# Kernel tuning notes

Hardware: AMD Instinct MI355X
Metric: run time of the kernel (lower is better)

Reference implementation:

```python
import jax, jax.numpy as jnp
import numpy as np

N = 50000      # nodes
E = 1600000    # edges (avg degree 32)
G = 128        # graphs in batch
NE = 5         # spectral supports (edge_attr channels)
NIN = 16       # input node features
H = 64         # nout1 hidden width
NCLS = 6
BN_EPS = 1e-5


def setup_inputs() -> dict:
    key = jax.random.key(0)
    ks = jax.random.split(key, 12)
    s = 0.1  # weight init scale
    x = jax.random.normal(ks[0], (N, NIN), dtype=jnp.float32)
    edge_index = jax.random.randint(ks[1], (2, E), 0, N, dtype=jnp.int32)
    edge_attr = jax.random.normal(ks[2], (E, NE), dtype=jnp.float32)
    # sorted segment ids covering all G graphs (non-empty segments)
    batch = ((jnp.arange(N, dtype=jnp.int32) * G) // N).astype(jnp.int32)
    W1 = jax.random.normal(ks[3], (NE, NIN, H), dtype=jnp.float32) * s
    W2 = jax.random.normal(ks[4], (NE, H, H), dtype=jnp.float32) * s
    W3 = jax.random.normal(ks[5], (NE, H, H), dtype=jnp.float32) * s
    W4 = jax.random.normal(ks[6], (NE, H, H), dtype=jnp.float32) * s
    b1 = jnp.zeros((H,), jnp.float32)
    b2 = jnp.zeros((H,), jnp.float32)
    b3 = jnp.zeros((H,), jnp.float32)
    b4 = jnp.zeros((H,), jnp.float32)
    bn_gamma = jnp.ones((2 * H,), jnp.float32)
    bn_beta = jnp.zeros((2 * H,), jnp.float32)
    bn_mean = jax.random.normal(ks[7], (2 * H,), dtype=jnp.float32)
    bn_var = jax.random.uniform(ks[8], (2 * H,), dtype=jnp.float32) + 0.5
    fc_w = jax.random.normal(ks[9], (2 * H, NCLS), dtype=jnp.float32) * s
    fc_b = jnp.zeros((NCLS,), jnp.float32)
    return {"x": x, "edge_index": edge_index, "edge_attr": edge_attr,
            "batch": batch, "W1": W1, "b1": b1, "W2": W2, "b2": b2,
            "W3": W3, "b3": b3, "W4": W4, "b4": b4,
            "bn_gamma": bn_gamma, "bn_beta": bn_beta,
            "bn_mean": bn_mean, "bn_var": bn_var,
            "fc_w": fc_w, "fc_b": fc_b}


def spect_conv(x, src, dst, edge_attr, W, b):
    # SpectConv(selfconn=False): out = sum_k scatter_add(edge_attr[:,k]*x[src] -> dst) @ W[k] + b
    xs = x[src]  # [E, F] gather
    n = x.shape[0]
    out = jnp.zeros((n, W.shape[2]), x.dtype)
    for k in range(W.shape[0]):  # K=5 spectral supports
        h = jax.ops.segment_sum(edge_attr[:, k:k + 1] * xs, dst, num_segments=n)
        out = out + h @ W[k]
    return out + b


def reference(x, edge_index, edge_attr, batch, W1, b1, W2, b2, W3, b3, W4, b4,
              bn_gamma, bn_beta, bn_mean, bn_var, fc_w, fc_b):
    src, dst = edge_index[0], edge_index[1]
    h = jax.nn.relu(spect_conv(x, src, dst, edge_attr, W1, b1))
    h = jax.nn.relu(spect_conv(h, src, dst, edge_attr, W2, b2))
    h = jax.nn.relu(spect_conv(h, src, dst, edge_attr, W3, b3))
    h = jax.nn.relu(spect_conv(h, src, dst, edge_attr, W4, b4))
    pooled = jnp.concatenate([
        jax.ops.segment_sum(h, batch, num_segments=G),
        jax.ops.segment_max(h, batch, num_segments=G)], axis=1)  # [G, 2H]
    bn = (pooled - bn_mean) * jax.lax.rsqrt(bn_var + BN_EPS) * bn_gamma + bn_beta
    return jax.nn.log_softmax(bn @ fc_w + fc_b, axis=1)
```

## Files before the change

### kernel.cpp

```cpp
#include <hip/hip_runtime.h>


#define Nn   50000
#define Ne   1600000
#define Gg   128
#define NEk  5
#define NINf 16
#define NCLSo 6
#define NB   196
#define RBK  128
#define CHK  (Ne / RBK)

using short8 = __attribute__((ext_vector_type(8))) short;
using f32x4  = __attribute__((ext_vector_type(4))) float;
using f32x2  = __attribute__((ext_vector_type(2))) float;
using uint4v = __attribute__((ext_vector_type(4))) unsigned;

__device__ __forceinline__ float2 bf2u(unsigned u) {
    return make_float2(__uint_as_float(u << 16), __uint_as_float(u & 0xffff0000u));
}
__device__ __forceinline__ unsigned f2bf(float a, float b) {
    unsigned ua = __float_as_uint(a), ub = __float_as_uint(b);
    ua += 0x7fffu + ((ua >> 16) & 1u);
    ub += 0x7fffu + ((ub >> 16) & 1u);
    return (ua >> 16) | (ub & 0xffff0000u);
}
__device__ __forceinline__ unsigned short f2bf1(float a) {
    unsigned ua = __float_as_uint(a);
    ua += 0x7fffu + ((ua >> 16) & 1u);
    return (unsigned short)(ua >> 16);
}

__device__ __forceinline__ f32x2 fma2s(float a, f32x2 x, f32x2 c) {
#if __has_builtin(__builtin_elementwise_fma)
    f32x2 av; av.x = a; av.y = a;
    return __builtin_elementwise_fma(av, x, c);
#else
    c.x = fmaf(a, x.x, c.x); c.y = fmaf(a, x.y, c.y);
    return c;
#endif
}


__global__ void k_pad_x(const float* __restrict__ x, unsigned* __restrict__ h0) {
    int i = blockIdx.x * 256 + threadIdx.x;
    if (i >= Nn * 32) return;
    int n = i >> 5, p = i & 31;
    int f0 = 2 * p;
    float v0 = (f0 < NINf) ? x[n * NINf + f0] : 0.f;
    float v1 = (f0 + 1 < NINf) ? x[n * NINf + f0 + 1] : 0.f;
    h0[i] = f2bf(v0, v1);
}

__global__ void k_pad_w1(const float* __restrict__ W1, float* __restrict__ W1p) {
    int i = blockIdx.x * 256 + threadIdx.x;
    if (i >= NEk * 64 * 64) return;
    int h = i & 63, f = (i >> 6) & 63, k = i >> 12;
    W1p[i] = (f < NINf) ? W1[(k * NINf + f) * 64 + h] : 0.f;
}

__global__ void k_pack_b(const float* __restrict__ W, unsigned short* __restrict__ bhi,
                         unsigned short* __restrict__ blo) {
    int i = blockIdx.x * 256 + threadIdx.x;
    if (i >= 20480) return;
    int j = i & 7, lane = (i >> 3) & 63, t2 = i >> 9;
    int nt = t2 / 10, kstep = t2 - nt * 10;
    int k = kstep * 32 + (lane >> 4) * 8 + j;
    int col = nt * 16 + (lane & 15);
    float v = W[k * 64 + col];
    unsigned short hi = f2bf1(v);
    float fhi = __uint_as_float(((unsigned)hi) << 16);
    bhi[i] = hi;
    blo[i] = f2bf1(v - fhi);
}

__global__ __launch_bounds__(1024) void k_rankhist(
    const int* __restrict__ ei, unsigned short* __restrict__ lrank,
    unsigned short* __restrict__ cnt ) {
    __shared__ unsigned hist[12500];
    int b = blockIdx.x, t = threadIdx.x;
    int e0 = b * CHK;
    for (int w = t; w < 12500; w += 1024) hist[w] = 0;
    __syncthreads();
    for (int i = t; i < CHK; i += 1024) {
        int d = ei[Ne + e0 + i];
        unsigned sh = 8u * (unsigned)(d & 3);
        unsigned old = atomicAdd(&hist[d >> 2], 1u << sh);
        lrank[e0 + i] = (unsigned short)((old >> sh) & 0xffu);
    }
    __syncthreads();
    unsigned* co = (unsigned*)(cnt + (size_t)b * Nn);
    for (int w = t; w < 12500; w += 1024) {
        unsigned hv = hist[w];
        co[2 * w]     = (hv & 0xffu) | ((hv >> 8) & 0xffu) << 16;
        co[2 * w + 1] = ((hv >> 16) & 0xffu) | (hv >> 24) << 16;
    }
}

__global__ void k_colscan(unsigned short* __restrict__ cnt, int* __restrict__ deg) {
    int d = blockIdx.x * 256 + threadIdx.x;
    if (d >= Nn) return;
    int s = 0;
#pragma unroll 4
    for (int b = 0; b < RBK; ++b) {
        int t = cnt[(size_t)b * Nn + d];
        cnt[(size_t)b * Nn + d] = (unsigned short)s;
        s += t;
    }
    deg[d] = s;
}


__global__ void k_blocksum(const int* __restrict__ deg, int* __restrict__ bsum) {
    __shared__ int l[256];
    int t = threadIdx.x;
    int i = blockIdx.x * 256 + t;
    l[t] = (i < Nn) ? deg[i] : 0;
    __syncthreads();
    for (int off = 128; off > 0; off >>= 1) {
        if (t < off) l[t] += l[t + off];
        __syncthreads();
    }
    if (t == 0) bsum[blockIdx.x] = l[0];
}

__global__ void k_scanpart(const int* __restrict__ bsum, int* __restrict__ boff) {
    __shared__ int l[256];
    int t = threadIdx.x;
    int v = (t < NB) ? bsum[t] : 0;
    l[t] = v;
    __syncthreads();
    for (int off = 1; off < 256; off <<= 1) {
        int u = (t >= off) ? l[t - off] : 0;
        __syncthreads();
        l[t] += u;
        __syncthreads();
    }
    if (t < NB) boff[t] = l[t] - v;
}

__global__ void k_scanfinal(const int* __restrict__ deg, const int* __restrict__ boff,
                            int* __restrict__ rowstart) {
    __shared__ int l[256];
    int t = threadIdx.x;
    int i = blockIdx.x * 256 + t;
    int v = (i < Nn) ? deg[i] : 0;
    l[t] = v;
    __syncthreads();
    for (int off = 1; off < 256; off <<= 1) {
        int u = (t >= off) ? l[t - off] : 0;
        __syncthreads();
        l[t] += u;
        __syncthreads();
    }
    if (i <= Nn) rowstart[i] = boff[blockIdx.x] + l[t] - v;
}

__global__ __launch_bounds__(256) void k_place(
    const int* __restrict__ ei, const float* __restrict__ eattr,
    const int* __restrict__ rowstart,
    const unsigned short* __restrict__ lrank,
    const unsigned short* __restrict__ cnt,
    unsigned* __restrict__ recs ) {
    int e = (blockIdx.x * 256 + threadIdx.x) * 4;
    if (e >= Ne) return;
    int b = e / CHK;
    const unsigned short* cb = cnt + (size_t)b * Nn;

    int4 dv = *(const int4*)(ei + Ne + e);
    int4 sv = *(const int4*)(ei + e);
    ushort4 lr = *(const ushort4*)(lrank + e);
    union { float4 v4[5]; float f[20]; } a;
#pragma unroll
    for (int q = 0; q < 5; ++q) a.v4[q] = *(const float4*)(eattr + (size_t)e * 5 + q * 4);

    int d[4] = { dv.x, dv.y, dv.z, dv.w };
    int s[4] = { sv.x, sv.y, sv.z, sv.w };
    unsigned short r4[4] = { lr.x, lr.y, lr.z, lr.w };
    int pos[4];
#pragma unroll
    for (int j = 0; j < 4; ++j)
        pos[j] = rowstart[d[j]] + cb[d[j]] + r4[j];
#pragma unroll
    for (int j = 0; j < 4; ++j) {
        uint4v rr;
        rr.x = (unsigned)s[j];
        rr.y = f2bf(a.f[5 * j],     a.f[5 * j + 1]);
        rr.z = f2bf(a.f[5 * j + 2], a.f[5 * j + 3]);
        rr.w = f2bf(a.f[5 * j + 4], 0.f);
        __builtin_nontemporal_store(rr, (uint4v*)(recs + (size_t)pos[j] * 4));
    }
}

__global__ void k_bounds(const int* __restrict__ batch, int* __restrict__ sg,
                         int* __restrict__ eg) {
    int n = blockIdx.x * 256 + threadIdx.x;
    if (n >= Nn) return;
    int g = batch[n];
    if (n == 0) sg[g] = 0;
    else {
        int gp = batch[n - 1];
        if (gp != g) { sg[g] = n; eg[gp] = n; }
    }
    if (n == Nn - 1) eg[g] = Nn;
}

#define SPAD 41
__global__ __launch_bounds__(256) void k_layer32(
    const unsigned* __restrict__ hin, const int* __restrict__ rowstart,
    const uint4* __restrict__ recs, const unsigned short* __restrict__ bhi,
    const unsigned short* __restrict__ blo, const float* __restrict__ bias,
    unsigned* __restrict__ outh) {
    __shared__ uint4 smem[32 * SPAD];
    unsigned* aggw = (unsigned*)smem;
    int t = threadIdx.x;
    int lane = t & 63, wave = t >> 6;
    int l = lane & 31, half = lane >> 5;
    int blk = blockIdx.x;

#pragma unroll 1
    for (int ni = 0; ni < 8; ++ni) {
        int row = wave * 8 + ni;
        int node = blk * 32 + row;
        if (node >= Nn) node = Nn - 1;
        node = __builtin_amdgcn_readfirstlane(node);
        int beg = rowstart[node], end = rowstart[node + 1];
        f32x2 c0 = {0.f, 0.f}, c1 = c0, c2 = c0, c3 = c0, c4 = c0;
        int ee = beg;
#define EDGE(E) { \
    uint4 r = recs[(E)]; \
    unsigned hx = hin[(size_t)(int)r.x * 32 + l]; \
    f32x2 xv; xv.x = __uint_as_float(hx << 16); xv.y = __uint_as_float(hx & 0xffff0000u); \
    float A0 = __uint_as_float(r.y << 16), A1 = __uint_as_float(r.y & 0xffff0000u); \
    float A2 = __uint_as_float(r.z << 16), A3 = __uint_as_float(r.z & 0xffff0000u); \
    float A4 = __uint_as_float(r.w << 16); \
    c0 = fma2s(A0, xv, c0); c1 = fma2s(A1, xv, c1); \
    c2 = fma2s(A2, xv, c2); c3 = fma2s(A3, xv, c3); \
    c4 = fma2s(A4, xv, c4); }
        for (; ee + 8 <= end; ee += 8) {
            EDGE(ee + half) EDGE(ee + 2 + half) EDGE(ee + 4 + half) EDGE(ee + 6 + half)
        }
        for (; ee + 2 <= end; ee += 2) { EDGE(ee + half) }
        if (ee < end) { if (half == 0) { EDGE(ee) } }
#undef EDGE
        c0.x += __shfl(c0.x, lane ^ 32); c0.y += __shfl(c0.y, lane ^ 32);
        c1.x += __shfl(c1.x, lane ^ 32); c1.y += __shfl(c1.y, lane ^ 32);
        c2.x += __shfl(c2.x, lane ^ 32); c2.y += __shfl(c2.y, lane ^ 32);
        c3.x += __shfl(c3.x, lane ^ 32); c3.y += __shfl(c3.y, lane ^ 32);
        c4.x += __shfl(c4.x, lane ^ 32); c4.y += __shfl(c4.y, lane ^ 32);
        if (half == 0) {
            unsigned* o = aggw + row * (SPAD * 4) + l;
            o[0]   = f2bf(c0.x, c0.y);
            o[32]  = f2bf(c1.x, c1.y);
            o[64]  = f2bf(c2.x, c2.y);
            o[96]  = f2bf(c3.x, c3.y);
            o[128] = f2bf(c4.x, c4.y);
        }
    }
    __syncthreads();

    int m = lane & 15, quad = lane >> 4;
    f32x4 acc0 = {0.f, 0.f, 0.f, 0.f}, acc1 = acc0;
    const uint4* ar0 = smem + m * SPAD + quad;
    const uint4* ar1 = smem + (16 + m) * SPAD + quad;
    const size_t bbase = (size_t)wave * 5120;
#pragma unroll 2
    for (int ks = 0; ks < 10; ++ks) {
        short8 a0 = *(const short8*)(ar0 + ks * 4);
        short8 a1 = *(const short8*)(ar1 + ks * 4);
        size_t bb = bbase + ((size_t)ks * 64 + lane) * 8;
        short8 h = *(const short8*)(bhi + bb);
        short8 lo = *(const short8*)(blo + bb);
        acc0 = __builtin_amdgcn_mfma_f32_16x16x32_bf16(a0, h,  acc0, 0, 0, 0);
        acc0 = __builtin_amdgcn_mfma_f32_16x16x32_bf16(a0, lo, acc0, 0, 0, 0);
        acc1 = __builtin_amdgcn_mfma_f32_16x16x32_bf16(a1, h,  acc1, 0, 0, 0);
        acc1 = __builtin_amdgcn_mfma_f32_16x16x32_bf16(a1, lo, acc1, 0, 0, 0);
    }
    __syncthreads();

    float* Cs = (float*)smem;
#pragma unroll
    for (int r = 0; r < 4; ++r) {
        int base = (quad * 4 + r) * 72 + wave * 16 + m;
        Cs[base]            = acc0[r];
        Cs[base + 16 * 72]  = acc1[r];
    }
    __syncthreads();

    {
        int row = t >> 3, grp = t & 7;
        int node = blk * 32 + row;
        if (node < Nn) {
            const float* cr = Cs + row * 72;
            unsigned o[4];
#pragma unroll
            for (int j = 0; j < 4; ++j) {
                int pp = grp * 4 + j;
                float v0 = fmaxf(cr[2 * pp]     + bias[2 * pp],     0.f);
                float v1 = fmaxf(cr[2 * pp + 1] + bias[2 * pp + 1], 0.f);
                o[j] = f2bf(v0, v1);
            }
            *(uint4*)(outh + (size_t)node * 32 + grp * 4) =
                make_uint4(o[0], o[1], o[2], o[3]);
        }
    }
}


__global__ __launch_bounds__(256) void k_pool(const unsigned* __restrict__ h,
                                              const int* __restrict__ sg,
                                              const int* __restrict__ eg,
                                              float* __restrict__ pooled) {
    __shared__ float2 ls[256], lm[256];
    int g = blockIdx.x, t = threadIdx.x;
    int p = t & 31, q = t >> 5;
    int s = sg[g], e = eg[g];
    float2 sum = {0.f, 0.f}, mx = {0.f, 0.f};
    for (int n = s + q; n < e; n += 8) {
        float2 v = bf2u(h[(size_t)n * 32 + p]);
        sum.x += v.x; sum.y += v.y;
        mx.x = fmaxf(mx.x, v.x); mx.y = fmaxf(mx.y, v.y);
    }
    ls[t] = sum; lm[t] = mx;
    __syncthreads();
    if (t < 32) {
        float2 ss = ls[t], mm = lm[t];
        for (int i = 1; i < 8; ++i) {
            float2 a = ls[t + i * 32], b = lm[t + i * 32];
            ss.x += a.x; ss.y += a.y;
            mm.x = fmaxf(mm.x, b.x); mm.y = fmaxf(mm.y, b.y);
        }
        pooled[g * 128 + 2 * t]          = ss.x;
        pooled[g * 128 + 2 * t + 1]      = ss.y;
        pooled[g * 128 + 64 + 2 * t]     = mm.x;
        pooled[g * 128 + 64 + 2 * t + 1] = mm.y;
    }
}

__global__ void k_head(const float* __restrict__ pooled, const float* __restrict__ gamma,
                       const float* __restrict__ beta, const float* __restrict__ mean,
                       const float* __restrict__ var, const float* __restrict__ fcw,
                       const float* __restrict__ fcb, float* __restrict__ out) {
    __shared__ float y[128];
    __shared__ float lg[8];
    int g = blockIdx.x, c = threadIdx.x;
    float p = pooled[g * 128 + c];
    y[c] = (p - mean[c]) * rsqrtf(var[c] + 1e-5f) * gamma[c] + beta[c];
    __syncthreads();
    if (c < NCLSo) {
        float l = fcb[c];
        for (int i = 0; i < 128; ++i) l += y[i] * fcw[i * NCLSo + c];
        lg[c] = l;
    }
    __syncthreads();
    if (c == 0) {
        float m = lg[0];
        for (int j = 1; j < NCLSo; ++j) m = fmaxf(m, lg[j]);
        float se = 0.f;
        for (int j = 0; j < NCLSo; ++j) se += expf(lg[j] - m);
        float lse = m + logf(se);
        for (int j = 0; j < NCLSo; ++j) out[g * NCLSo + j] = lg[j] - lse;
    }
}


static inline size_t rup(size_t x) { return (x + 255) & ~(size_t)255; }

extern "C" void kernel_launch(void* const* d_in, const int* in_sizes, int n_in,
                              void* d_out, int out_size, void* d_ws, size_t ws_size,
                              hipStream_t stream) {
    const float* x     = (const float*)d_in[0];
    const int*   ei    = (const int*)d_in[1];
    const float* eattr = (const float*)d_in[2];
    const int*   batch = (const int*)d_in[3];
    const float* W1    = (const float*)d_in[4];
    const float* b1    = (const float*)d_in[5];
    const float* W2    = (const float*)d_in[6];
    const float* b2    = (const float*)d_in[7];
    const float* W3    = (const float*)d_in[8];
    const float* b3    = (const float*)d_in[9];
    const float* W4    = (const float*)d_in[10];
    const float* b4    = (const float*)d_in[11];
    const float* gamma = (const float*)d_in[12];
    const float* beta  = (const float*)d_in[13];
    const float* mean  = (const float*)d_in[14];
    const float* var   = (const float*)d_in[15];
    const float* fcw   = (const float*)d_in[16];
    const float* fcb   = (const float*)d_in[17];
    float* out = (float*)d_out;

    char* p = (char*)d_ws;
    auto take = [&](size_t bytes) { char* r = p; p += rup(bytes); return r; };
    int*            deg      = (int*)take((size_t)(Nn + 1) * 4);
    unsigned short* cnt      = (unsigned short*)take((size_t)RBK * Nn * 2);
    unsigned short* lrank    = (unsigned short*)take((size_t)Ne * 2);
    int*            rowstart = (int*)take((size_t)(Nn + 1) * 4);
    int*            bsum     = (int*)take((size_t)NB * 4);
    int*            boff     = (int*)take((size_t)NB * 4);
    uint4*          recs     = (uint4*)take((size_t)Ne * 16);
    unsigned*       hA       = (unsigned*)take((size_t)Nn * 32 * 4);
    unsigned*       hB       = (unsigned*)take((size_t)Nn * 32 * 4);
    float*          W1p      = (float*)take((size_t)NEk * 64 * 64 * 4);
    unsigned short* bhiA     = (unsigned short*)take((size_t)4 * 20480 * 2);
    unsigned short* bloA     = (unsigned short*)take((size_t)4 * 20480 * 2);
    float*          pooled   = (float*)take((size_t)Gg * 128 * 4);
    int*            sg       = (int*)take((size_t)Gg * 4);
    int*            eg       = (int*)take((size_t)Gg * 4);

    k_rankhist<<<RBK, 1024, 0, stream>>>(ei, lrank, cnt);
    k_pad_x<<<(Nn * 32 + 255) / 256, 256, 0, stream>>>(x, hA);
    k_pad_w1<<<(NEk * 64 * 64 + 255) / 256, 256, 0, stream>>>(W1, W1p);
    k_pack_b<<<80, 256, 0, stream>>>(W1p, bhiA,             bloA);
    k_pack_b<<<80, 256, 0, stream>>>(W2,  bhiA + 20480,     bloA + 20480);
    k_pack_b<<<80, 256, 0, stream>>>(W3,  bhiA + 2 * 20480, bloA + 2 * 20480);
    k_pack_b<<<80, 256, 0, stream>>>(W4,  bhiA + 3 * 20480, bloA + 3 * 20480);
    k_colscan<<<NB, 256, 0, stream>>>(cnt, deg);
    k_blocksum<<<NB, 256, 0, stream>>>(deg, bsum);
    k_scanpart<<<1, 256, 0, stream>>>(bsum, boff);
    k_scanfinal<<<NB, 256, 0, stream>>>(deg, boff, rowstart);
    k_place<<<(Ne / 4 + 255) / 256, 256, 0, stream>>>(ei, eattr, rowstart, lrank, cnt,
                                                      (unsigned*)recs);
    k_bounds<<<(Nn + 255) / 256, 256, 0, stream>>>(batch, sg, eg);

    const float* bs[4] = { b1, b2, b3, b4 };
    unsigned* cur = hA;
    unsigned* nxt = hB;
    for (int L = 0; L < 4; ++L) {
        k_layer32<<<(Nn + 31) / 32, 256, 0, stream>>>(
            cur, rowstart, recs, bhiA + (size_t)L * 20480, bloA + (size_t)L * 20480,
            bs[L], nxt);
        unsigned* tmp = cur; cur = nxt; nxt = tmp;
    }

    k_pool<<<Gg, 256, 0, stream>>>(cur, sg, eg, pooled);
    k_head<<<Gg, 128, 0, stream>>>(pooled, gamma, beta, mean, var, fcw, fcb, out);
}
```

Baseline: 554.0 us.

## Split fused layer kernel into separate aggregate and transform kernels

Result: faster. 455.9 us (median of 2 runs) (-17.7%).

```diff
diff --git a/kernel.cpp b/kernel.cpp
--- a/kernel.cpp
+++ b/kernel.cpp
@@ -14,7 +14,6 @@
 using short8 = __attribute__((ext_vector_type(8))) short;
 using f32x4  = __attribute__((ext_vector_type(4))) float;
 using f32x2  = __attribute__((ext_vector_type(2))) float;
-using uint4v = __attribute__((ext_vector_type(4))) unsigned;
 
 __device__ __forceinline__ float2 bf2u(unsigned u) {
     return make_float2(__uint_as_float(u << 16), __uint_as_float(u & 0xffff0000u));
@@ -156,40 +155,23 @@
     if (i <= Nn) rowstart[i] = boff[blockIdx.x] + l[t] - v;
 }
 
-__global__ __launch_bounds__(256) void k_place(
-    const int* __restrict__ ei, const float* __restrict__ eattr,
-    const int* __restrict__ rowstart,
-    const unsigned short* __restrict__ lrank,
-    const unsigned short* __restrict__ cnt,
-    unsigned* __restrict__ recs ) {
-    int e = (blockIdx.x * 256 + threadIdx.x) * 4;
+__global__ void k_place(const int* __restrict__ ei, const float* __restrict__ eattr,
+                        const int* __restrict__ rowstart,
+                        const unsigned short* __restrict__ lrank,
+                        const unsigned short* __restrict__ cnt,
+                        uint4* __restrict__ recs) {
+    int e = blockIdx.x * 256 + threadIdx.x;
     if (e >= Ne) return;
+    int d = ei[Ne + e];
     int b = e / CHK;
-    const unsigned short* cb = cnt + (size_t)b * Nn;
-
-    int4 dv = *(const int4*)(ei + Ne + e);
-    int4 sv = *(const int4*)(ei + e);
-    ushort4 lr = *(const ushort4*)(lrank + e);
-    union { float4 v4[5]; float f[20]; } a;
-#pragma unroll
-    for (int q = 0; q < 5; ++q) a.v4[q] = *(const float4*)(eattr + (size_t)e * 5 + q * 4);
-
-    int d[4] = { dv.x, dv.y, dv.z, dv.w };
-    int s[4] = { sv.x, sv.y, sv.z, sv.w };
-    unsigned short r4[4] = { lr.x, lr.y, lr.z, lr.w };
-    int pos[4];
-#pragma unroll
-    for (int j = 0; j < 4; ++j)
-        pos[j] = rowstart[d[j]] + cb[d[j]] + r4[j];
-#pragma unroll
-    for (int j = 0; j < 4; ++j) {
-        uint4v rr;
-        rr.x = (unsigned)s[j];
-        rr.y = f2bf(a.f[5 * j],     a.f[5 * j + 1]);
-        rr.z = f2bf(a.f[5 * j + 2], a.f[5 * j + 3]);
-        rr.w = f2bf(a.f[5 * j + 4], 0.f);
-        __builtin_nontemporal_store(rr, (uint4v*)(recs + (size_t)pos[j] * 4));
-    }
+    int pos = rowstart[d] + cnt[(size_t)b * Nn + d] + lrank[e];
+    const float* a = eattr + (size_t)e * 5;
+    uint4 rr;
+    rr.x = (unsigned)ei[e];
+    rr.y = f2bf(a[0], a[1]);
+    rr.z = f2bf(a[2], a[3]);
+    rr.w = f2bf(a[4], 0.f);
+    recs[pos] = rr;
 }
 
 __global__ void k_bounds(const int* __restrict__ batch, int* __restrict__ sg,
@@ -205,28 +187,16 @@
     if (n == Nn - 1) eg[g] = Nn;
 }
 
-#define SPAD 41
-__global__ __launch_bounds__(256) void k_layer32(
+
+__global__ __launch_bounds__(256) void k_aggregate(
     const unsigned* __restrict__ hin, const int* __restrict__ rowstart,
-    const uint4* __restrict__ recs, const unsigned short* __restrict__ bhi,
-    const unsigned short* __restrict__ blo, const float* __restrict__ bias,
-    unsigned* __restrict__ outh) {
-    __shared__ uint4 smem[32 * SPAD];
-    unsigned* aggw = (unsigned*)smem;
-    int t = threadIdx.x;
-    int lane = t & 63, wave = t >> 6;
+    const uint4* __restrict__ recs, unsigned* __restrict__ agg) {
+    int lane = threadIdx.x & 63;
     int l = lane & 31, half = lane >> 5;
-    int blk = blockIdx.x;
-
-#pragma unroll 1
-    for (int ni = 0; ni < 8; ++ni) {
-        int row = wave * 8 + ni;
-        int node = blk * 32 + row;
-        if (node >= Nn) node = Nn - 1;
-        node = __builtin_amdgcn_readfirstlane(node);
-        int beg = rowstart[node], end = rowstart[node + 1];
-        f32x2 c0 = {0.f, 0.f}, c1 = c0, c2 = c0, c3 = c0, c4 = c0;
-        int ee = beg;
+    int node = __builtin_amdgcn_readfirstlane((int)(blockIdx.x * 4 + (threadIdx.x >> 6)));
+    int beg = rowstart[node], end = rowstart[node + 1];
+    f32x2 c0 = {0.f, 0.f}, c1 = c0, c2 = c0, c3 = c0, c4 = c0;
+    int ee = beg;
 #define EDGE(E) { \
     uint4 r = recs[(E)]; \
     unsigned hx = hin[(size_t)(int)r.x * 32 + l]; \
@@ -237,29 +207,48 @@
     c0 = fma2s(A0, xv, c0); c1 = fma2s(A1, xv, c1); \
     c2 = fma2s(A2, xv, c2); c3 = fma2s(A3, xv, c3); \
     c4 = fma2s(A4, xv, c4); }
-        for (; ee + 8 <= end; ee += 8) {
-            EDGE(ee + half) EDGE(ee + 2 + half) EDGE(ee + 4 + half) EDGE(ee + 6 + half)
-        }
-        for (; ee + 2 <= end; ee += 2) { EDGE(ee + half) }
-        if (ee < end) { if (half == 0) { EDGE(ee) } }
+    for (; ee + 8 <= end; ee += 8) {
+        EDGE(ee + half) EDGE(ee + 2 + half) EDGE(ee + 4 + half) EDGE(ee + 6 + half)
+    }
+    for (; ee + 2 <= end; ee += 2) { EDGE(ee + half) }
+    if (ee < end) { if (half == 0) { EDGE(ee) } }
 #undef EDGE
-        c0.x += __shfl(c0.x, lane ^ 32); c0.y += __shfl(c0.y, lane ^ 32);
-        c1.x += __shfl(c1.x, lane ^ 32); c1.y += __shfl(c1.y, lane ^ 32);
-        c2.x += __shfl(c2.x, lane ^ 32); c2.y += __shfl(c2.y, lane ^ 32);
-        c3.x += __shfl(c3.x, lane ^ 32); c3.y += __shfl(c3.y, lane ^ 32);
-        c4.x += __shfl(c4.x, lane ^ 32); c4.y += __shfl(c4.y, lane ^ 32);
-        if (half == 0) {
-            unsigned* o = aggw + row * (SPAD * 4) + l;
-            o[0]   = f2bf(c0.x, c0.y);
-            o[32]  = f2bf(c1.x, c1.y);
-            o[64]  = f2bf(c2.x, c2.y);
-            o[96]  = f2bf(c3.x, c3.y);
-            o[128] = f2bf(c4.x, c4.y);
-        }
-    }
-    __syncthreads();
-
+    c0.x += __shfl(c0.x, lane ^ 32); c0.y += __shfl(c0.y, lane ^ 32);
+    c1.x += __shfl(c1.x, lane ^ 32); c1.y += __shfl(c1.y, lane ^ 32);
+    c2.x += __shfl(c2.x, lane ^ 32); c2.y += __shfl(c2.y, lane ^ 32);
+    c3.x += __shfl(c3.x, lane ^ 32); c3.y += __shfl(c3.y, lane ^ 32);
+    c4.x += __shfl(c4.x, lane ^ 32); c4.y += __shfl(c4.y, lane ^ 32);
+    if (half == 0) {
+        unsigned* o = agg + (size_t)node * 160 + l;
+        o[0]   = f2bf(c0.x, c0.y);
+        o[32]  = f2bf(c1.x, c1.y);
+        o[64]  = f2bf(c2.x, c2.y);
+        o[96]  = f2bf(c3.x, c3.y);
+        o[128] = f2bf(c4.x, c4.y);
+    }
+}
+
+#define SPAD 41
+__global__ __launch_bounds__(256) void k_transform(
+    const uint4* __restrict__ A, const unsigned short* __restrict__ bhi,
+    const unsigned short* __restrict__ blo, const float* __restrict__ bias,
+    unsigned* __restrict__ outh) {
+    __shared__ uint4 smem[32 * SPAD];
+    int t = threadIdx.x;
+    int lane = t & 63, wave = t >> 6;
     int m = lane & 15, quad = lane >> 4;
+    int blk = blockIdx.x;
+
+#pragma unroll
+    for (int it = 0; it < 5; ++it) {
+        int v = t + it * 256;
+        int row = v / 40, off = v - row * 40;
+        int node = blk * 32 + row;
+        if (node >= Nn) node = Nn - 1;
+        smem[row * SPAD + off] = A[(size_t)node * 40 + off];
+    }
+    __syncthreads();
+
     f32x4 acc0 = {0.f, 0.f, 0.f, 0.f}, acc1 = acc0;
     const uint4* ar0 = smem + m * SPAD + quad;
     const uint4* ar1 = smem + (16 + m) * SPAD + quad;
@@ -400,6 +389,7 @@
     uint4*          recs     = (uint4*)take((size_t)Ne * 16);
     unsigned*       hA       = (unsigned*)take((size_t)Nn * 32 * 4);
     unsigned*       hB       = (unsigned*)take((size_t)Nn * 32 * 4);
+    unsigned*       agg      = (unsigned*)take((size_t)Nn * 160 * 4);
     float*          W1p      = (float*)take((size_t)NEk * 64 * 64 * 4);
     unsigned short* bhiA     = (unsigned short*)take((size_t)4 * 20480 * 2);
     unsigned short* bloA     = (unsigned short*)take((size_t)4 * 20480 * 2);
@@ -418,16 +408,16 @@
     k_blocksum<<<NB, 256, 0, stream>>>(deg, bsum);
     k_scanpart<<<1, 256, 0, stream>>>(bsum, boff);
     k_scanfinal<<<NB, 256, 0, stream>>>(deg, boff, rowstart);
-    k_place<<<(Ne / 4 + 255) / 256, 256, 0, stream>>>(ei, eattr, rowstart, lrank, cnt,
-                                                      (unsigned*)recs);
+    k_place<<<(Ne + 255) / 256, 256, 0, stream>>>(ei, eattr, rowstart, lrank, cnt, recs);
     k_bounds<<<(Nn + 255) / 256, 256, 0, stream>>>(batch, sg, eg);
 
     const float* bs[4] = { b1, b2, b3, b4 };
     unsigned* cur = hA;
     unsigned* nxt = hB;
     for (int L = 0; L < 4; ++L) {
-        k_layer32<<<(Nn + 31) / 32, 256, 0, stream>>>(
-            cur, rowstart, recs, bhiA + (size_t)L * 20480, bloA + (size_t)L * 20480,
+        k_aggregate<<<Nn / 4, 256, 0, stream>>>(cur, rowstart, recs, agg);
+        k_transform<<<(Nn + 31) / 32, 256, 0, stream>>>(
+            (const uint4*)agg, bhiA + (size_t)L * 20480, bloA + (size_t)L * 20480,
             bs[L], nxt);
         unsigned* tmp = cur; cur = nxt; nxt = tmp;
     }
```
